# Performance work log

Hardware: AMD Instinct MI355X
Metric: run time of the kernel (lower is better)

## Reference

```python
import jax, jax.numpy as jnp
import numpy as np

N_NODES = 100000
N_EDGES = 1600000
IN_RAW = 64
HID = 128


def setup_inputs() -> dict:
    key = jax.random.key(0)
    ks = jax.random.split(key, 16)
    inp = {
        "x": jax.random.normal(ks[0], (N_NODES, IN_RAW), dtype=jnp.float32),
        "edge_index": jax.random.randint(ks[1], (2, N_EDGES), 0, N_NODES, dtype=jnp.int64),
        "user_ids": jax.random.randint(ks[2], (N_NODES,), 0, 10000, dtype=jnp.int64),
        "locations": jax.random.randint(ks[3], (N_NODES,), 0, 1000, dtype=jnp.int64),
        "time_features": jax.random.normal(ks[4], (N_NODES, 4), dtype=jnp.float32),
        # embeddings / encoders
        "user_emb_table": jax.random.normal(ks[5], (10000, 32), dtype=jnp.float32) * 0.02,
        "loc_emb_table": jax.random.normal(ks[6], (1000, 16), dtype=jnp.float32) * 0.02,
        "W_time": jax.random.normal(ks[7], (4, 16), dtype=jnp.float32) * 0.1,
        "b_time": jnp.zeros((16,), dtype=jnp.float32),
        # SAGEConv 1: lin_l (aggregated, with bias), lin_r (root, no bias)
        "W1_l": jax.random.normal(ks[8], (HID, HID), dtype=jnp.float32) * (1.0 / np.sqrt(HID)),
        "b1": jnp.zeros((HID,), dtype=jnp.float32),
        "W1_r": jax.random.normal(ks[9], (HID, HID), dtype=jnp.float32) * (1.0 / np.sqrt(HID)),
        # SAGEConv 2
        "W2_l": jax.random.normal(ks[10], (HID, HID), dtype=jnp.float32) * (1.0 / np.sqrt(HID)),
        "b2": jnp.zeros((HID,), dtype=jnp.float32),
        "W2_r": jax.random.normal(ks[11], (HID, HID), dtype=jnp.float32) * (1.0 / np.sqrt(HID)),
        # classifier
        "Wc": jax.random.normal(ks[12], (HID, 1), dtype=jnp.float32) * (1.0 / np.sqrt(HID)),
        "bc": jnp.zeros((1,), dtype=jnp.float32),
    }
    return inp


def _sage_conv(h, src, dst, W_l, b_l, W_r, n_nodes):
    # mean aggregation of source features onto targets (PyG SAGEConv default)
    msg_sum = jax.ops.segment_sum(h[src], dst, num_segments=n_nodes)  # [N, D]
    deg = jax.ops.segment_sum(jnp.ones((src.shape[0],), h.dtype), dst, num_segments=n_nodes)
    agg = msg_sum / jnp.maximum(deg, 1.0)[:, None]
    return agg @ W_l + b_l + h @ W_r


def reference(x, edge_index, user_ids, locations, time_features,
              user_emb_table, loc_emb_table, W_time, b_time,
              W1_l, b1, W1_r, W2_l, b2, W2_r, Wc, bc):
    n = x.shape[0]
    src, dst = edge_index[0], edge_index[1]
    user_emb = user_emb_table[user_ids]            # [N, 32]
    loc_emb = loc_emb_table[locations]             # [N, 16]
    time_emb = time_features @ W_time + b_time     # [N, 16]
    h = jnp.concatenate([x, user_emb, loc_emb, time_emb], axis=-1)  # [N, 128]
    h = jax.nn.relu(_sage_conv(h, src, dst, W1_l, b1, W1_r, n))  # dropout = identity (eval)
    h = jax.nn.relu(_sage_conv(h, src, dst, W2_l, b2, W2_r, n))
    return jax.nn.sigmoid(h @ Wc + bc)  # [N, 1]
```

## Files before the change

### kernel.cpp

```cpp
#include <hip/hip_runtime.h>
#include <math.h>

#define N_NODES 100000
#define HID 128
#define NB 782
#define CAP 4096
#define NBLK 256
#define BTILE 6250
#define SUBCAP 32
#define SCAP 3072
#define WPB 32
#define EBLK 3125

typedef __attribute__((ext_vector_type(8))) short bf16x8;
typedef __attribute__((ext_vector_type(4))) float f32x4;
typedef __attribute__((ext_vector_type(2))) float f32x2;

__device__ __forceinline__ unsigned short f2bf(float f) {
  union { float f; unsigned u; } v; v.f = f;
  unsigned r = v.u + 0x7FFFu + ((v.u >> 16) & 1u);
  return (unsigned short)(r >> 16);
}
__device__ __forceinline__ unsigned packbf(float lo, float hi) {
  return (unsigned)f2bf(lo) | ((unsigned)f2bf(hi) << 16);
}
__device__ __forceinline__ unsigned pkfp8x4(float a, float b, float c, float d) {
  int v = __builtin_amdgcn_cvt_pk_fp8_f32(a, b, 0, false);
  v = __builtin_amdgcn_cvt_pk_fp8_f32(c, d, v, true);
  return (unsigned)v;
}
__device__ __forceinline__ float bflo(unsigned u) {
  union { unsigned u; float f; } v; v.u = u << 16; return v.f;
}
__device__ __forceinline__ float bfhi(unsigned u) {
  union { unsigned u; float f; } v; v.u = u & 0xFFFF0000u; return v.f;
}
__device__ __forceinline__ void acc_add_fp8(float* a, unsigned w) {
  f32x2 p0 = __builtin_amdgcn_cvt_pk_f32_fp8((int)w, false);
  f32x2 p1 = __builtin_amdgcn_cvt_pk_f32_fp8((int)w, true);
  a[0] += p0.x; a[1] += p0.y; a[2] += p1.x; a[3] += p1.y;
}
__device__ __forceinline__ void acc_add_row(float* a, uint4 u) {
  acc_add_fp8(a + 0, u.x);
  acc_add_fp8(a + 4, u.y);
  acc_add_fp8(a + 8, u.z);
  acc_add_fp8(a + 12, u.w);
}

__global__ __launch_bounds__(512) void k_bktembed(
    const int* __restrict__ src, const int* __restrict__ dst,
    int* __restrict__ gcnt, unsigned* __restrict__ bdata2, int E,
    const float* __restrict__ x, const int* __restrict__ uid,
    const int* __restrict__ lid, const float* __restrict__ timef,
    const float* __restrict__ utab, const float* __restrict__ ltab,
    const float* __restrict__ Wt, const float* __restrict__ bt,
    unsigned short* __restrict__ h0, unsigned char* __restrict__ h0f8) {
  __shared__ int hcnt[NB];
  int t = threadIdx.x;
  if (blockIdx.x < NBLK) {
    int blk = blockIdx.x;
    int e0 = blk * BTILE;
    int e1 = min(e0 + BTILE, E);
    for (int i = t; i < NB; i += 512) hcnt[i] = 0;
    __syncthreads();
#pragma unroll 4
    for (int e = e0 + t; e < e1; e += 512) {
      int d = dst[e], s = src[e];
      int b = d >> 7;
      int pos = atomicAdd(&hcnt[b], 1);
      if (pos < SUBCAP)
        bdata2[((size_t)blk * NB + b) * SUBCAP + pos] =
            ((unsigned)s << 7) | (unsigned)(d & 127);
    }
    __syncthreads();
    for (int i = t; i < NB; i += 512)
      gcnt[blk * NB + i] = hcnt[i];
    return;
  }
  int v = (blockIdx.x - NBLK) * 32 + (t >> 4);
  int g = t & 15;
  if (v >= N_NODES) return;
  float val[8];
  if (g < 8) {
    const float4* xp = (const float4*)&x[(size_t)v * 64 + g * 8];
    float4 a = xp[0], b = xp[1];
    val[0] = a.x; val[1] = a.y; val[2] = a.z; val[3] = a.w;
    val[4] = b.x; val[5] = b.y; val[6] = b.z; val[7] = b.w;
  } else if (g < 12) {
    const float4* up = (const float4*)&utab[(size_t)uid[v] * 32 + (g - 8) * 8];
    float4 a = up[0], b = up[1];
    val[0] = a.x; val[1] = a.y; val[2] = a.z; val[3] = a.w;
    val[4] = b.x; val[5] = b.y; val[6] = b.z; val[7] = b.w;
  } else if (g < 14) {
    const float4* lp = (const float4*)&ltab[(size_t)lid[v] * 16 + (g - 12) * 8];
    float4 a = lp[0], b = lp[1];
    val[0] = a.x; val[1] = a.y; val[2] = a.z; val[3] = a.w;
    val[4] = b.x; val[5] = b.y; val[6] = b.z; val[7] = b.w;
  } else {
    int c0 = (g - 14) * 8;
    float4 tf = *(const float4*)&timef[(size_t)v * 4];
#pragma unroll
    for (int i = 0; i < 8; ++i) {
      int c = c0 + i;
      val[i] = bt[c] + tf.x * Wt[c] + tf.y * Wt[16 + c] + tf.z * Wt[32 + c] +
               tf.w * Wt[48 + c];
    }
  }
  uint4 ob;
  ob.x = packbf(val[0], val[1]);
  ob.y = packbf(val[2], val[3]);
  ob.z = packbf(val[4], val[5]);
  ob.w = packbf(val[6], val[7]);
  *(uint4*)&h0[(size_t)v * 128 + g * 8] = ob;
  uint2 of;
  of.x = pkfp8x4(val[0], val[1], val[2], val[3]);
  of.y = pkfp8x4(val[4], val[5], val[6], val[7]);
  *(uint2*)&h0f8[(size_t)v * 128 + g * 8] = of;
}

__global__ __launch_bounds__(512) void k_bfill(
    const int* __restrict__ gcnt, const unsigned* __restrict__ bdata2,
    int* __restrict__ rstart, int* __restrict__ rdeg, int* __restrict__ col,
    const float* __restrict__ W1l, const float* __restrict__ W1r,
    const float* __restrict__ W2l, const float* __restrict__ W2r,
    unsigned short* __restrict__ WT) {
  int b = blockIdx.x;
  int t = threadIdx.x;
  if (b >= NB) {
    int lin = ((b - NB) * 512 + t) * 4;
    int m = lin >> 14;
    int rem = lin & 16383;
    int f = rem >> 7;
    int k0 = rem & 127;
    const float* W = (m == 0) ? W1l : (m == 1) ? W1r : (m == 2) ? W2l : W2r;
    unsigned short o[4];
#pragma unroll
    for (int j = 0; j < 4; ++j) o[j] = f2bf(W[(size_t)(k0 + j) * 128 + f]);
    uint2 pk;
    pk.x = (unsigned)o[0] | ((unsigned)o[1] << 16);
    pk.y = (unsigned)o[2] | ((unsigned)o[3] << 16);
    *(uint2*)&WT[m * 16384 + f * 128 + k0] = pk;
    return;
  }
  __shared__ unsigned sdata[SCAP];
  __shared__ int soff[NBLK];
  __shared__ int scnt[NBLK];
  __shared__ int wsum[8];
  __shared__ int lcnt[128];
  __shared__ int wtot;
  int lane = t & 63, wv = t >> 6;

  int c = (t < NBLK) ? min(gcnt[t * NB + b], SUBCAP) : 0;
  int x = c;
#pragma unroll
  for (int off = 1; off < 64; off <<= 1) {
    int v = __shfl_up(x, off);
    if (lane >= off) x += v;
  }
  if (lane == 63) wsum[wv] = x;
  __syncthreads();
  int add = 0;
#pragma unroll
  for (int k = 0; k < 8; ++k)
    if (k < wv) add += wsum[k];
  x += add;
  int tot = 0;
#pragma unroll
  for (int k = 0; k < 4; ++k) tot += wsum[k];
  tot = min(tot, SCAP);
  if (t < NBLK) { soff[t] = x - c; scnt[t] = c; }
  if (t < 128) lcnt[t] = 0;
  __syncthreads();

  for (int i = t; i < NBLK * 8; i += 512) {
    int j = i >> 3, p4 = (i & 7) * 4;
    int cj = scnt[j];
    if (p4 < cj) {
      uint4 v = *(const uint4*)&bdata2[((size_t)j * NB + b) * SUBCAP + p4];
      int bs = soff[j] + p4;
      int n = min(4, cj - p4);
      unsigned vv[4] = {v.x, v.y, v.z, v.w};
#pragma unroll
      for (int e = 0; e < 4; ++e)
        if (e < n && bs + e < SCAP) sdata[bs + e] = vv[e];
    }
  }
  __syncthreads();

  for (int i = t; i < tot; i += 512) atomicAdd(&lcnt[sdata[i] & 127u], 1);
  __syncthreads();

  int node0 = b * 128;
  int base = b * CAP;
  if (t < 128) {
    int cc = lcnt[t];
    int xx = cc;
#pragma unroll
    for (int off = 1; off < 64; off <<= 1) {
      int v = __shfl_up(xx, off);
      if (lane >= off) xx += v;
    }
    if (t == 63) wtot = xx;
    __syncthreads();
    if (t >= 64) xx += wtot;
    int excl = xx - cc;
    if (node0 + t < N_NODES) {
      rstart[node0 + t] = base + excl;
      rdeg[node0 + t] = cc;
    }
    lcnt[t] = excl;
  } else {
    __syncthreads();
  }
  __syncthreads();
  for (int i = t; i < tot; i += 512) {
    unsigned v = sdata[i];
    int pos = base + atomicAdd(&lcnt[v & 127u], 1);
    col[pos] = (int)(v >> 7);
  }
}

template <bool CLS>
__global__ __launch_bounds__(256, 4) void k_aggemm(
    const unsigned char* __restrict__ hf8, const int* __restrict__ rstart,
    const int* __restrict__ rdeg, const int* __restrict__ col,
    const unsigned short* __restrict__ hin,
    const unsigned short* __restrict__ WlT, const unsigned short* __restrict__ WrT,
    const float* __restrict__ bias, unsigned short* __restrict__ hout,
    unsigned char* __restrict__ houtf8,
    const float* __restrict__ Wc, const float* __restrict__ bc,
    float* __restrict__ out) {
  __shared__ unsigned short SB[2 * 64 * 136];
  __shared__ int wk;
  unsigned short* As = SB;
  unsigned short* Hs = SB + 64 * 136;
  unsigned short* Ot = SB;
  float* zred = (float*)SB;
  int t = threadIdx.x;
  int lane = t & 63;
  int wave = t >> 6;
  int wn = wave * 32;
  int l15 = lane & 15;
  int quad = lane >> 4;
  int mbase = blockIdx.x * 64;

  int sr = t >> 2, sseg = t & 3;
  uint4 hv[4];
  {
    int gn = mbase + sr;
    if (gn < N_NODES) {
      const uint4* hp = (const uint4*)(hin + (size_t)gn * 128 + sseg * 32);
#pragma unroll
      for (int i = 0; i < 4; ++i) hv[i] = hp[i];
    } else {
#pragma unroll
      for (int i = 0; i < 4; ++i) hv[i] = make_uint4(0, 0, 0, 0);
    }
  }
  if (t == 0) wk = 0;
  __syncthreads();

  const uint4* h8 = (const uint4*)hf8;
  int q = t & 7;
  int gbase = lane & 56;
  for (;;) {
    int myn = 0;
    if (q == 0) myn = atomicAdd(&wk, 1);
    myn = __shfl(myn, gbase);
    if (myn >= 64) break;
    int v = mbase + myn;
    float acc[16];
#pragma unroll
    for (int i = 0; i < 16; ++i) acc[i] = 0.f;
    float inv = 0.f;
    if (v < N_NODES) {
      int s0 = rstart[v];
      int deg = rdeg[v];
      int s1 = s0 + deg;
      int j = s0;
      for (; j + 4 <= s1; j += 4) {
        uint4 r0 = h8[(size_t)col[j] * 8 + q];
        uint4 r1 = h8[(size_t)col[j + 1] * 8 + q];
        uint4 r2 = h8[(size_t)col[j + 2] * 8 + q];
        uint4 r3 = h8[(size_t)col[j + 3] * 8 + q];
        acc_add_row(acc, r0);
        acc_add_row(acc, r1);
        acc_add_row(acc, r2);
        acc_add_row(acc, r3);
      }
      for (; j < s1; ++j) acc_add_row(acc, h8[(size_t)col[j] * 8 + q]);
      inv = 1.f / (float)(deg > 0 ? deg : 1);
    }
    uint4 o0, o1;
    o0.x = packbf(acc[0] * inv, acc[1] * inv);
    o0.y = packbf(acc[2] * inv, acc[3] * inv);
    o0.z = packbf(acc[4] * inv, acc[5] * inv);
    o0.w = packbf(acc[6] * inv, acc[7] * inv);
    o1.x = packbf(acc[8] * inv, acc[9] * inv);
    o1.y = packbf(acc[10] * inv, acc[11] * inv);
    o1.z = packbf(acc[12] * inv, acc[13] * inv);
    o1.w = packbf(acc[14] * inv, acc[15] * inv);
    *(uint4*)&As[myn * 136 + q * 16] = o0;
    *(uint4*)&As[myn * 136 + q * 16 + 8] = o1;
  }

#pragma unroll
  for (int i = 0; i < 4; ++i)
    *(uint4*)&Hs[sr * 136 + sseg * 32 + i * 8] = hv[i];
  __syncthreads();

  f32x4 acc4[4][2];
#pragma unroll
  for (int i = 0; i < 4; ++i)
#pragma unroll
    for (int j = 0; j < 2; ++j) acc4[i][j] = (f32x4){0.f, 0.f, 0.f, 0.f};

#pragma unroll
  for (int ks = 0; ks < 4; ++ks) {
    int kb = ks * 32 + quad * 8;
    bf16x8 bL[2], bR[2];
#pragma unroll
    for (int jn = 0; jn < 2; ++jn) {
      int f = wn + jn * 16 + l15;
      bL[jn] = *(const bf16x8*)&WlT[(size_t)f * 128 + kb];
      bR[jn] = *(const bf16x8*)&WrT[(size_t)f * 128 + kb];
    }
    bf16x8 aA[4], aH[4];
#pragma unroll
    for (int im = 0; im < 4; ++im) {
      aA[im] = *(const bf16x8*)&As[(im * 16 + l15) * 136 + kb];
      aH[im] = *(const bf16x8*)&Hs[(im * 16 + l15) * 136 + kb];
    }
#pragma unroll
    for (int im = 0; im < 4; ++im)
#pragma unroll
      for (int jn = 0; jn < 2; ++jn)
        acc4[im][jn] = __builtin_amdgcn_mfma_f32_16x16x32_bf16(
            aA[im], bL[jn], acc4[im][jn], 0, 0, 0);
#pragma unroll
    for (int im = 0; im < 4; ++im)
#pragma unroll
      for (int jn = 0; jn < 2; ++jn)
        acc4[im][jn] = __builtin_amdgcn_mfma_f32_16x16x32_bf16(
            aH[im], bR[jn], acc4[im][jn], 0, 0, 0);
  }

  float bv[2];
#pragma unroll
  for (int jn = 0; jn < 2; ++jn) bv[jn] = bias[wn + jn * 16 + l15];

  __syncthreads();

  if (!CLS) {
#pragma unroll
    for (int im = 0; im < 4; ++im)
#pragma unroll
      for (int rr = 0; rr < 4; ++rr) {
        int rloc = im * 16 + quad * 4 + rr;
#pragma unroll
        for (int jn = 0; jn < 2; ++jn)
          Ot[rloc * 136 + wn + jn * 16 + l15] =
              f2bf(fmaxf(acc4[im][jn][rr] + bv[jn], 0.f));
      }
    __syncthreads();
    int r = t >> 2, seg = t & 3;
    int node = mbase + r;
    if (node < N_NODES) {
      uint4 d0[4];
      const uint4* srcp = (const uint4*)&Ot[r * 136 + seg * 32];
      uint4* dstp = (uint4*)&hout[(size_t)node * 128 + seg * 32];
#pragma unroll
      for (int i = 0; i < 4; ++i) { d0[i] = srcp[i]; dstp[i] = d0[i]; }
      unsigned w[8];
#pragma unroll
      for (int i = 0; i < 4; ++i) {
        unsigned u[4] = {d0[i].x, d0[i].y, d0[i].z, d0[i].w};
#pragma unroll
        for (int p = 0; p < 2; ++p) {
          w[i * 2 + p] = pkfp8x4(bflo(u[p * 2]), bfhi(u[p * 2]),
                                 bflo(u[p * 2 + 1]), bfhi(u[p * 2 + 1]));
        }
      }
      uint4* fp = (uint4*)&houtf8[(size_t)node * 128 + seg * 32];
      fp[0] = make_uint4(w[0], w[1], w[2], w[3]);
      fp[1] = make_uint4(w[4], w[5], w[6], w[7]);
    }
  } else {
    float wcv[2];
#pragma unroll
    for (int jn = 0; jn < 2; ++jn) wcv[jn] = Wc[wn + jn * 16 + l15];
#pragma unroll
    for (int im = 0; im < 4; ++im) {
#pragma unroll
      for (int rr = 0; rr < 4; ++rr) {
        float p = 0.f;
#pragma unroll
        for (int jn = 0; jn < 2; ++jn)
          p += fmaxf(acc4[im][jn][rr] + bv[jn], 0.f) * wcv[jn];
        p += __shfl_xor(p, 1);
        p += __shfl_xor(p, 2);
        p += __shfl_xor(p, 4);
        p += __shfl_xor(p, 8);
        if (l15 == 0) zred[wave * 64 + im * 16 + quad * 4 + rr] = p;
      }
    }
    __syncthreads();
    if (t < 64) {
      int node = mbase + t;
      if (node < N_NODES) {
        float z = zred[t] + zred[64 + t] + zred[128 + t] + zred[192 + t] + bc[0];
        out[node] = 1.f / (1.f + expf(-z));
      }
    }
  }
}

extern "C" void kernel_launch(void* const* d_in, const int* in_sizes, int n_in,
                              void* d_out, int out_size, void* d_ws, size_t ws_size,
                              hipStream_t stream) {
  const float* x     = (const float*)d_in[0];
  const int*   eidx  = (const int*)d_in[1];
  const int*   uid   = (const int*)d_in[2];
  const int*   lid   = (const int*)d_in[3];
  const float* timef = (const float*)d_in[4];
  const float* utab  = (const float*)d_in[5];
  const float* ltab  = (const float*)d_in[6];
  const float* Wt    = (const float*)d_in[7];
  const float* bt    = (const float*)d_in[8];
  const float* W1l   = (const float*)d_in[9];
  const float* b1    = (const float*)d_in[10];
  const float* W1r   = (const float*)d_in[11];
  const float* W2l   = (const float*)d_in[12];
  const float* b2    = (const float*)d_in[13];
  const float* W2r   = (const float*)d_in[14];
  const float* Wc    = (const float*)d_in[15];
  const float* bc    = (const float*)d_in[16];
  float* out = (float*)d_out;

  const int E = in_sizes[1] / 2;
  const int* src = eidx;
  const int* dst = eidx + E;

  char* ws = (char*)d_ws;
  size_t off = 0;
  auto alloc = [&](size_t bytes) -> void* {
    void* p = ws + off;
    off += (bytes + 255) & ~(size_t)255;
    return p;
  };
  const size_t HBYTES = (size_t)N_NODES * 128 * sizeof(unsigned short);
  const size_t FBYTES = (size_t)N_NODES * 128;
  unsigned short* h0  = (unsigned short*)alloc(HBYTES);
  unsigned short* h1  = (unsigned short*)alloc(HBYTES);
  unsigned char* h0f8 = (unsigned char*)alloc(FBYTES);
  unsigned char* h1f8 = (unsigned char*)alloc(FBYTES);
  unsigned short* WT  = (unsigned short*)alloc(4 * 16384 * sizeof(unsigned short));
  unsigned* bdata2    = (unsigned*)alloc((size_t)NBLK * NB * SUBCAP * 4);
  int* gcnt           = (int*)alloc((size_t)NBLK * NB * 4);
  int* col            = (int*)alloc((size_t)NB * CAP * 4);
  int* rstart         = (int*)alloc((size_t)N_NODES * 4);
  int* rdeg           = (int*)alloc((size_t)N_NODES * 4);
  (void)ws_size; (void)n_in; (void)out_size;

  k_bktembed<<<NBLK + EBLK, 512, 0, stream>>>(src, dst, gcnt, bdata2, E,
                                              x, uid, lid, timef, utab, ltab,
                                              Wt, bt, h0, h0f8);
  k_bfill<<<NB + WPB, 512, 0, stream>>>(gcnt, bdata2, rstart, rdeg, col,
                                        W1l, W1r, W2l, W2r, WT);

  k_aggemm<false><<<(N_NODES + 63) / 64, 256, 0, stream>>>(
      h0f8, rstart, rdeg, col, h0, WT, WT + 16384, b1, h1, h1f8,
      nullptr, nullptr, nullptr);

  k_aggemm<true><<<(N_NODES + 63) / 64, 256, 0, stream>>>(
      h1f8, rstart, rdeg, col, h1, WT + 32768, WT + 49152, b2,
      nullptr, nullptr, Wc, bc, out);
}
```

Measured before the change: 264.4 us.

## Shrink aggregate-GEMM tile to 32 nodes and drop dynamic work queue

The fused aggregation+GEMM kernel now handles 32 nodes per 256-thread block instead of 64. Each group of 8 threads is bound statically to one node, replacing the LDS atomic work-stealing loop and its extra barrier. This halves LDS use per block and doubles the grid, which should raise occupancy and latency hiding on the irregular gather. The cost is no load balancing across skewed degrees within a block, and each block now reloads the full weight matrices for half as many rows.

```diff
diff --git a/kernel.cpp b/kernel.cpp
--- a/kernel.cpp
+++ b/kernel.cpp
@@ -230,10 +230,9 @@
     unsigned char* __restrict__ houtf8,
     const float* __restrict__ Wc, const float* __restrict__ bc,
     float* __restrict__ out) {
-  __shared__ unsigned short SB[2 * 64 * 136];
-  __shared__ int wk;
+  __shared__ unsigned short SB[2 * 32 * 136];
   unsigned short* As = SB;
-  unsigned short* Hs = SB + 64 * 136;
+  unsigned short* Hs = SB + 32 * 136;
   unsigned short* Ot = SB;
   float* zred = (float*)SB;
   int t = threadIdx.x;
@@ -242,33 +241,24 @@
   int wn = wave * 32;
   int l15 = lane & 15;
   int quad = lane >> 4;
-  int mbase = blockIdx.x * 64;
-
-  int sr = t >> 2, sseg = t & 3;
-  uint4 hv[4];
+  int mbase = blockIdx.x * 32;
+
+  int r = t >> 3, q = t & 7;
+
+  uint4 hv[2];
   {
-    int gn = mbase + sr;
+    int gn = mbase + r;
     if (gn < N_NODES) {
-      const uint4* hp = (const uint4*)(hin + (size_t)gn * 128 + sseg * 32);
-#pragma unroll
-      for (int i = 0; i < 4; ++i) hv[i] = hp[i];
+      const uint4* hp = (const uint4*)(hin + (size_t)gn * 128 + q * 16);
+      hv[0] = hp[0]; hv[1] = hp[1];
     } else {
-#pragma unroll
-      for (int i = 0; i < 4; ++i) hv[i] = make_uint4(0, 0, 0, 0);
-    }
-  }
-  if (t == 0) wk = 0;
-  __syncthreads();
-
-  const uint4* h8 = (const uint4*)hf8;
-  int q = t & 7;
-  int gbase = lane & 56;
-  for (;;) {
-    int myn = 0;
-    if (q == 0) myn = atomicAdd(&wk, 1);
-    myn = __shfl(myn, gbase);
-    if (myn >= 64) break;
-    int v = mbase + myn;
+      hv[0] = make_uint4(0, 0, 0, 0); hv[1] = make_uint4(0, 0, 0, 0);
+    }
+  }
+
+  {
+    const uint4* h8 = (const uint4*)hf8;
+    int v = mbase + r;
     float acc[16];
 #pragma unroll
     for (int i = 0; i < 16; ++i) acc[i] = 0.f;
@@ -300,18 +290,17 @@
     o1.y = packbf(acc[10] * inv, acc[11] * inv);
     o1.z = packbf(acc[12] * inv, acc[13] * inv);
     o1.w = packbf(acc[14] * inv, acc[15] * inv);
-    *(uint4*)&As[myn * 136 + q * 16] = o0;
-    *(uint4*)&As[myn * 136 + q * 16 + 8] = o1;
-  }
-
-#pragma unroll
-  for (int i = 0; i < 4; ++i)
-    *(uint4*)&Hs[sr * 136 + sseg * 32 + i * 8] = hv[i];
-  __syncthreads();
-
-  f32x4 acc4[4][2];
-#pragma unroll
-  for (int i = 0; i < 4; ++i)
+    *(uint4*)&As[r * 136 + q * 16] = o0;
+    *(uint4*)&As[r * 136 + q * 16 + 8] = o1;
+  }
+
+  *(uint4*)&Hs[r * 136 + q * 16] = hv[0];
+  *(uint4*)&Hs[r * 136 + q * 16 + 8] = hv[1];
+  __syncthreads();
+
+  f32x4 acc4[2][2];
+#pragma unroll
+  for (int i = 0; i < 2; ++i)
 #pragma unroll
     for (int j = 0; j < 2; ++j) acc4[i][j] = (f32x4){0.f, 0.f, 0.f, 0.f};
 
@@ -325,20 +314,20 @@
       bL[jn] = *(const bf16x8*)&WlT[(size_t)f * 128 + kb];
       bR[jn] = *(const bf16x8*)&WrT[(size_t)f * 128 + kb];
     }
-    bf16x8 aA[4], aH[4];
-#pragma unroll
-    for (int im = 0; im < 4; ++im) {
+    bf16x8 aA[2], aH[2];
+#pragma unroll
+    for (int im = 0; im < 2; ++im) {
       aA[im] = *(const bf16x8*)&As[(im * 16 + l15) * 136 + kb];
       aH[im] = *(const bf16x8*)&Hs[(im * 16 + l15) * 136 + kb];
     }
 #pragma unroll
-    for (int im = 0; im < 4; ++im)
+    for (int im = 0; im < 2; ++im)
 #pragma unroll
       for (int jn = 0; jn < 2; ++jn)
         acc4[im][jn] = __builtin_amdgcn_mfma_f32_16x16x32_bf16(
             aA[im], bL[jn], acc4[im][jn], 0, 0, 0);
 #pragma unroll
-    for (int im = 0; im < 4; ++im)
+    for (int im = 0; im < 2; ++im)
 #pragma unroll
       for (int jn = 0; jn < 2; ++jn)
         acc4[im][jn] = __builtin_amdgcn_mfma_f32_16x16x32_bf16(
@@ -353,7 +342,7 @@
 
   if (!CLS) {
 #pragma unroll
-    for (int im = 0; im < 4; ++im)
+    for (int im = 0; im < 2; ++im)
 #pragma unroll
       for (int rr = 0; rr < 4; ++rr) {
         int rloc = im * 16 + quad * 4 + rr;
@@ -363,17 +352,16 @@
               f2bf(fmaxf(acc4[im][jn][rr] + bv[jn], 0.f));
       }
     __syncthreads();
-    int r = t >> 2, seg = t & 3;
     int node = mbase + r;
     if (node < N_NODES) {
-      uint4 d0[4];
-      const uint4* srcp = (const uint4*)&Ot[r * 136 + seg * 32];
-      uint4* dstp = (uint4*)&hout[(size_t)node * 128 + seg * 32];
-#pragma unroll
-      for (int i = 0; i < 4; ++i) { d0[i] = srcp[i]; dstp[i] = d0[i]; }
-      unsigned w[8];
-#pragma unroll
-      for (int i = 0; i < 4; ++i) {
+      uint4 d0[2];
+      const uint4* srcp = (const uint4*)&Ot[r * 136 + q * 16];
+      uint4* dstp = (uint4*)&hout[(size_t)node * 128 + q * 16];
+      d0[0] = srcp[0]; d0[1] = srcp[1];
+      dstp[0] = d0[0]; dstp[1] = d0[1];
+      unsigned w[4];
+#pragma unroll
+      for (int i = 0; i < 2; ++i) {
         unsigned u[4] = {d0[i].x, d0[i].y, d0[i].z, d0[i].w};
 #pragma unroll
         for (int p = 0; p < 2; ++p) {
@@ -381,16 +369,15 @@
                                  bflo(u[p * 2 + 1]), bfhi(u[p * 2 + 1]));
         }
       }
-      uint4* fp = (uint4*)&houtf8[(size_t)node * 128 + seg * 32];
-      fp[0] = make_uint4(w[0], w[1], w[2], w[3]);
-      fp[1] = make_uint4(w[4], w[5], w[6], w[7]);
+      *(uint4*)&houtf8[(size_t)node * 128 + q * 16] =
+          make_uint4(w[0], w[1], w[2], w[3]);
     }
   } else {
     float wcv[2];
 #pragma unroll
     for (int jn = 0; jn < 2; ++jn) wcv[jn] = Wc[wn + jn * 16 + l15];
 #pragma unroll
-    for (int im = 0; im < 4; ++im) {
+    for (int im = 0; im < 2; ++im) {
 #pragma unroll
       for (int rr = 0; rr < 4; ++rr) {
         float p = 0.f;
@@ -401,14 +388,14 @@
         p += __shfl_xor(p, 2);
         p += __shfl_xor(p, 4);
         p += __shfl_xor(p, 8);
-        if (l15 == 0) zred[wave * 64 + im * 16 + quad * 4 + rr] = p;
+        if (l15 == 0) zred[wave * 32 + im * 16 + quad * 4 + rr] = p;
       }
     }
     __syncthreads();
-    if (t < 64) {
+    if (t < 32) {
       int node = mbase + t;
       if (node < N_NODES) {
-        float z = zred[t] + zred[64 + t] + zred[128 + t] + zred[192 + t] + bc[0];
+        float z = zred[t] + zred[32 + t] + zred[64 + t] + zred[96 + t] + bc[0];
         out[node] = 1.f / (1.f + expf(-z));
       }
     }
@@ -468,11 +455,11 @@
   k_bfill<<<NB + WPB, 512, 0, stream>>>(gcnt, bdata2, rstart, rdeg, col,
                                         W1l, W1r, W2l, W2r, WT);
 
-  k_aggemm<false><<<(N_NODES + 63) / 64, 256, 0, stream>>>(
+  k_aggemm<false><<<(N_NODES + 31) / 32, 256, 0, stream>>>(
       h0f8, rstart, rdeg, col, h0, WT, WT + 16384, b1, h1, h1f8,
       nullptr, nullptr, nullptr);
 
-  k_aggemm<true><<<(N_NODES + 63) / 64, 256, 0, stream>>>(
+  k_aggemm<true><<<(N_NODES + 31) / 32, 256, 0, stream>>>(
       h1f8, rstart, rdeg, col, h1, WT + 32768, WT + 49152, b2,
       nullptr, nullptr, Wc, bc, out);
 }
```

Result: slower. 274.4 us (+3.8%).
